# Performance work log

Measured on AMD Instinct MI355X. Metric: run time of the kernel, lower is better.

## Reference

```python
import jax, jax.numpy as jnp
import numpy as np

B, N, D, ATT = 8, 2048, 1024, 128

def setup_inputs() -> dict:
    key = jax.random.key(0)
    k1, k2, k3 = jax.random.split(key, 3)
    s = 1.0 / np.sqrt(D)
    return {
        "x": jax.random.normal(k1, (B, N, D), dtype=jnp.float32),
        "Wf": jax.random.normal(k2, (D, ATT), dtype=jnp.float32) * s,
        "bf": jnp.zeros((ATT,), dtype=jnp.float32),
        "Wg": jax.random.normal(k3, (D, ATT), dtype=jnp.float32) * s,
        "bg": jnp.zeros((ATT,), dtype=jnp.float32),
    }

def reference(x, Wf, bf, Wg, bg):
    # f, g: [B, N, ATT]
    f = jnp.einsum('bnd,da->bna', x, Wf) + bf
    g = jnp.einsum('bnd,da->bna', x, Wg) + bg
    # unscaled attention logits [B, N, N]
    att = jnp.einsum('bna,bma->bnm', f, g)
    att = jax.nn.softmax(att, axis=-1)
    # NOTE: original multiplies attention with x (not h); h branch is dead code.
    out = jnp.einsum('bnm,bmd->bnd', att, x)
    return out + x  # residual=True
```

## Files before the change

kernel.cpp:

```cpp
#include <hip/hip_runtime.h>
#include <hip/hip_fp16.h>


#define B_ 8
#define N_ 2048
#define D_ 1024
#define A_ 128

typedef _Float16 half8v  __attribute__((ext_vector_type(8)));
typedef _Float16 half4v  __attribute__((ext_vector_type(4)));
typedef float    floatx4 __attribute__((ext_vector_type(4)));

__device__ __forceinline__ floatx4 mfma32(half8v a, half8v b, floatx4 c) {
#if defined(__HIP_DEVICE_COMPILE__)
    return __builtin_amdgcn_mfma_f32_16x16x32_f16(a, b, c, 0, 0, 0);
#else
    return c;
#endif
}

__global__ __launch_bounds__(256) void xpose_kernel(
    const float* __restrict__ x, _Float16* __restrict__ xT)
{
    __shared__ __align__(16) _Float16 ts[64][80];
    const int n0 = blockIdx.x * 64, d0 = blockIdx.y * 64, b = blockIdx.z;
    const int t = threadIdx.x;
#pragma unroll
    for (int s = 0; s < 4; ++s) {
        int idx = t + 256 * s;
        int nl = idx >> 4, c4 = idx & 15;
        float4 v = ((const float4*)(x + ((size_t)(b * N_ + n0 + nl)) * D_ + d0))[c4];
        ts[c4 * 4 + 0][nl] = (_Float16)v.x;
        ts[c4 * 4 + 1][nl] = (_Float16)v.y;
        ts[c4 * 4 + 2][nl] = (_Float16)v.z;
        ts[c4 * 4 + 3][nl] = (_Float16)v.w;
    }
    __syncthreads();
#pragma unroll
    for (int s = 0; s < 2; ++s) {
        int idx = t + 256 * s;
        int dl = idx >> 3, c = idx & 7;
        *(uint4*)&xT[((size_t)b * D_ + d0 + dl) * N_ + n0 + c * 8] =
            *(const uint4*)&ts[dl][c * 8];
    }
}

__global__ __launch_bounds__(256) void wprep_kernel(
    const float* __restrict__ Wf, const float* __restrict__ Wg,
    _Float16* __restrict__ whT)
{
    __shared__ __align__(16) _Float16 ts[64][72];
    const int k0 = blockIdx.x * 64, c0 = blockIdx.y * 64;
    const float* W = blockIdx.z ? Wg : Wf;
    _Float16* dst = whT + (size_t)blockIdx.z * A_ * D_;
    const int t = threadIdx.x;
#pragma unroll
    for (int s = 0; s < 4; ++s) {
        int idx = t + 256 * s;
        int kl = idx >> 4, c4 = idx & 15;
        float4 v = *(const float4*)&W[(size_t)(k0 + kl) * A_ + c0 + c4 * 4];
        ts[c4 * 4 + 0][kl] = (_Float16)v.x;
        ts[c4 * 4 + 1][kl] = (_Float16)v.y;
        ts[c4 * 4 + 2][kl] = (_Float16)v.z;
        ts[c4 * 4 + 3][kl] = (_Float16)v.w;
    }
    __syncthreads();
#pragma unroll
    for (int s = 0; s < 2; ++s) {
        int idx = t + 256 * s;
        int cl = idx >> 3, ch = idx & 7;
        *(uint4*)&dst[(size_t)(c0 + cl) * D_ + k0 + ch * 8] =
            *(const uint4*)&ts[cl][ch * 8];
    }
}

__global__ __launch_bounds__(256) void fgmm_kernel(
    const float* __restrict__ x, const _Float16* __restrict__ whT,
    const float* __restrict__ bfv, const float* __restrict__ bgv,
    _Float16* __restrict__ fh, _Float16* __restrict__ gh)
{
    __shared__ __align__(16) _Float16 xs[64 * 40];
    __shared__ __align__(16) _Float16 wt[256 * 40];
    const int row0 = blockIdx.x * 64;
    const int t = threadIdx.x;
    const int w = t >> 6, lane = t & 63, quad = lane >> 4, l16 = lane & 15;
    const int wr  = (w >> 1) * 32;
    const int wch = (w & 1);

    float4 xRf[2];
    uint4  wR[4];
#define FG_LOAD_TILE(K0)                                                      \
    {                                                                         \
        _Pragma("unroll")                                                     \
        for (int s = 0; s < 2; ++s) {                                         \
            int idx = t + 256 * s;                                            \
            int r = idx >> 3, k4 = idx & 7;                                   \
            xRf[s] = *(const float4*)&x[(size_t)(row0 + r) * D_ + (K0) + k4 * 4]; \
        }                                                                     \
        _Pragma("unroll")                                                     \
        for (int s = 0; s < 4; ++s) {                                         \
            int idx = t + 256 * s;                                            \
            int c = idx >> 2, k8 = idx & 3;                                   \
            wR[s] = *(const uint4*)&whT[(size_t)c * D_ + (K0) + k8 * 8];      \
        }                                                                     \
    }

    FG_LOAD_TILE(0)

    floatx4 acc[2][8];
#pragma unroll
    for (int ms = 0; ms < 2; ++ms)
#pragma unroll
        for (int nt = 0; nt < 8; ++nt)
            acc[ms][nt] = (floatx4){0.f, 0.f, 0.f, 0.f};

    for (int kt = 0; kt < 32; ++kt) {
        __syncthreads();
#pragma unroll
        for (int s = 0; s < 2; ++s) {
            int idx = t + 256 * s;
            int r = idx >> 3, k4 = idx & 7;
            half4v h = {(_Float16)xRf[s].x, (_Float16)xRf[s].y,
                        (_Float16)xRf[s].z, (_Float16)xRf[s].w};
            *(half4v*)&xs[r * 40 + k4 * 4] = h;
        }
#pragma unroll
        for (int s = 0; s < 4; ++s) {
            int idx = t + 256 * s;
            int c = idx >> 2, k8 = idx & 3;
            *(uint4*)&wt[c * 40 + k8 * 8] = wR[s];
        }
        __syncthreads();
        if (kt < 31) FG_LOAD_TILE((kt + 1) * 32)

        half8v a0 = *(const half8v*)&xs[(wr + l16) * 40 + quad * 8];
        half8v a1 = *(const half8v*)&xs[(wr + 16 + l16) * 40 + quad * 8];
#pragma unroll
        for (int nt = 0; nt < 8; ++nt) {
            half8v bfr = *(const half8v*)&wt[(wch * 128 + nt * 16 + l16) * 40 + quad * 8];
            acc[0][nt] = mfma32(a0, bfr, acc[0][nt]);
            acc[1][nt] = mfma32(a1, bfr, acc[1][nt]);
        }
    }

    _Float16* dst = wch ? gh : fh;
    const float* bias = wch ? bgv : bfv;
#pragma unroll
    for (int nt = 0; nt < 8; ++nt) {
        int col = nt * 16 + l16;
        float bv = bias[col];
#pragma unroll
        for (int ms = 0; ms < 2; ++ms)
#pragma unroll
            for (int rg = 0; rg < 4; ++rg) {
                int row = row0 + wr + ms * 16 + quad * 4 + rg;
                dst[(size_t)row * A_ + col] = (_Float16)(acc[ms][nt][rg] + bv);
            }
    }
}

__global__ __launch_bounds__(256, 2) void attn_kernel(
    const float* __restrict__ x, const _Float16* __restrict__ f,
    const _Float16* __restrict__ g, const _Float16* __restrict__ xT,
    float* __restrict__ out)
{
    __shared__ __align__(16) _Float16 gS[32 * 136];
    __shared__ __align__(16) _Float16 xTs[256 * 40];

    const int dch = blockIdx.x;
    const int nt  = blockIdx.y;
    const int b   = blockIdx.z;
    const int tid = threadIdx.x;
    const int wave = tid >> 6, lane = tid & 63;
    const int quad = lane >> 4, l16 = lane & 15;
    const int d0 = dch * 256;
    const int qbase = nt * 128 + wave * 32;

    half8v fb[2][4];
#pragma unroll
    for (int it = 0; it < 2; ++it)
#pragma unroll
        for (int kc = 0; kc < 4; ++kc)
            fb[it][kc] = *(const half8v*)(f +
                ((size_t)(b * N_ + qbase + it * 16 + l16)) * A_ + kc * 32 + quad * 8);

    uint4 gR[2];
    uint2 xR[8];
#define AT_LOAD_TILE(M0)                                                      \
    {                                                                         \
        _Pragma("unroll")                                                     \
        for (int s = 0; s < 2; ++s) {                                         \
            int idx = tid + 256 * s;                                          \
            int r = idx >> 4, c = idx & 15;                                   \
            gR[s] = *(const uint4*)(g + ((size_t)(b * N_ + (M0) + r)) * A_ + c * 8); \
        }                                                                     \
        _Pragma("unroll")                                                     \
        for (int s = 0; s < 8; ++s) {                                         \
            int idx = tid + 256 * s;                                          \
            int rr = idx >> 3, p = idx & 7;                                   \
            xR[s] = *(const uint2*)(xT + ((size_t)b * D_ + d0 + rr) * N_ + (M0) + p * 4); \
        }                                                                     \
    }

    AT_LOAD_TILE(0)

    floatx4 acc[2][16];
#pragma unroll
    for (int it = 0; it < 2; ++it)
#pragma unroll
        for (int dt = 0; dt < 16; ++dt)
            acc[it][dt] = (floatx4){0.f, 0.f, 0.f, 0.f};
    float m_i[2]    = {-3.0e38f, -3.0e38f};
    float l_part[2] = {0.f, 0.f};

    for (int m0 = 0; m0 < N_; m0 += 32) {
        __syncthreads();
#pragma unroll
        for (int s = 0; s < 2; ++s) {
            int idx = tid + 256 * s;
            int r = idx >> 4, c = idx & 15;
            int slot = ((r >> 2) & 1) * 16 + ((r >> 3) & 3) * 4 + (r & 3);
            *(uint4*)&gS[slot * 136 + c * 8] = gR[s];
        }
#pragma unroll
        for (int s = 0; s < 8; ++s) {
            int idx = tid + 256 * s;
            int rr = idx >> 3, p = idx & 7;
            *(uint2*)&xTs[rr * 40 + p * 4] = xR[s];
        }
        __syncthreads();
        if (m0 + 32 < N_) AT_LOAD_TILE(m0 + 32)

        floatx4 sc[2][2];
#pragma unroll
        for (int fr = 0; fr < 2; ++fr)
#pragma unroll
            for (int it = 0; it < 2; ++it)
                sc[fr][it] = (floatx4){0.f, 0.f, 0.f, 0.f};
#pragma unroll
        for (int kc = 0; kc < 4; ++kc) {
            half8v ga0 = *(const half8v*)&gS[(l16     ) * 136 + kc * 32 + quad * 8];
            half8v ga1 = *(const half8v*)&gS[(l16 + 16) * 136 + kc * 32 + quad * 8];
            sc[0][0] = mfma32(ga0, fb[0][kc], sc[0][0]);
            sc[0][1] = mfma32(ga0, fb[1][kc], sc[0][1]);
            sc[1][0] = mfma32(ga1, fb[0][kc], sc[1][0]);
            sc[1][1] = mfma32(ga1, fb[1][kc], sc[1][1]);
        }

        float tm[2];
#pragma unroll
        for (int it = 0; it < 2; ++it) {
            float t0 = fmaxf(fmaxf(sc[0][it][0], sc[0][it][1]),
                             fmaxf(sc[0][it][2], sc[0][it][3]));
            float t1 = fmaxf(fmaxf(sc[1][it][0], sc[1][it][1]),
                             fmaxf(sc[1][it][2], sc[1][it][3]));
            float tv = fmaxf(t0, t1);
            tv = fmaxf(tv, __shfl_xor(tv, 16));
            tv = fmaxf(tv, __shfl_xor(tv, 32));
            tm[it] = tv;
        }
        bool needl = (tm[0] > m_i[0] + 8.0f) || (tm[1] > m_i[1] + 8.0f);
        if (__any(needl)) {
            float alpha[2];
#pragma unroll
            for (int it = 0; it < 2; ++it) {
                float mnew = fmaxf(m_i[it], tm[it]);
                alpha[it] = __expf(m_i[it] - mnew);
                m_i[it] = mnew;
                l_part[it] *= alpha[it];
            }
            float ar[2][4];
#pragma unroll
            for (int it = 0; it < 2; ++it)
#pragma unroll
                for (int r = 0; r < 4; ++r)
                    ar[it][r] = __shfl(alpha[it], quad * 4 + r);
#pragma unroll
            for (int it = 0; it < 2; ++it)
#pragma unroll
                for (int dt = 0; dt < 16; ++dt)
#pragma unroll
                    for (int r = 0; r < 4; ++r)
                        acc[it][dt][r] *= ar[it][r];
        }

        half8v pa[2];
#pragma unroll
        for (int it = 0; it < 2; ++it) {
            float e0 = __expf(sc[0][it][0] - m_i[it]);
            float e1 = __expf(sc[0][it][1] - m_i[it]);
            float e2 = __expf(sc[0][it][2] - m_i[it]);
            float e3 = __expf(sc[0][it][3] - m_i[it]);
            float e4 = __expf(sc[1][it][0] - m_i[it]);
            float e5 = __expf(sc[1][it][1] - m_i[it]);
            float e6 = __expf(sc[1][it][2] - m_i[it]);
            float e7 = __expf(sc[1][it][3] - m_i[it]);
            l_part[it] += ((e0 + e1) + (e2 + e3)) + ((e4 + e5) + (e6 + e7));
            pa[it] = (half8v){(_Float16)e0, (_Float16)e1, (_Float16)e2,
                              (_Float16)e3, (_Float16)e4, (_Float16)e5,
                              (_Float16)e6, (_Float16)e7};
        }

#pragma unroll
        for (int dt = 0; dt < 16; ++dt) {
            half8v xb = *(const half8v*)&xTs[(dt * 16 + l16) * 40 + quad * 8];
            acc[0][dt] = mfma32(pa[0], xb, acc[0][dt]);
            acc[1][dt] = mfma32(pa[1], xb, acc[1][dt]);
        }
    }

    float l_i[2];
#pragma unroll
    for (int it = 0; it < 2; ++it) {
        float rs = l_part[it];
        rs += __shfl_xor(rs, 16);
        rs += __shfl_xor(rs, 32);
        l_i[it] = rs;
    }
    float linv[2][4];
#pragma unroll
    for (int it = 0; it < 2; ++it)
#pragma unroll
        for (int r = 0; r < 4; ++r)
            linv[it][r] = 1.0f / __shfl(l_i[it], quad * 4 + r);

#pragma unroll
    for (int it = 0; it < 2; ++it)
#pragma unroll
        for (int r = 0; r < 4; ++r) {
            const size_t rowoff =
                ((size_t)(b * N_ + qbase + it * 16 + quad * 4 + r)) * D_ + d0;
#pragma unroll
            for (int dt = 0; dt < 16; ++dt) {
                int col = dt * 16 + l16;
                out[rowoff + col] = fmaf(acc[it][dt][r], linv[it][r], x[rowoff + col]);
            }
        }
}

extern "C" void kernel_launch(void* const* d_in, const int* in_sizes, int n_in,
                              void* d_out, int out_size, void* d_ws, size_t ws_size,
                              hipStream_t stream) {
    const float* x   = (const float*)d_in[0];
    const float* Wf  = (const float*)d_in[1];
    const float* bfv = (const float*)d_in[2];
    const float* Wg  = (const float*)d_in[3];
    const float* bgv = (const float*)d_in[4];
    float* out = (float*)d_out;

    _Float16* fh  = (_Float16*)d_ws;
    _Float16* gh  = fh + (size_t)B_ * N_ * A_;
    _Float16* xT  = gh + (size_t)B_ * N_ * A_;
    _Float16* whT = xT + (size_t)B_ * D_ * N_;

    hipLaunchKernelGGL(xpose_kernel, dim3(N_ / 64, D_ / 64, B_), dim3(256), 0, stream,
                       x, xT);
    hipLaunchKernelGGL(wprep_kernel, dim3(D_ / 64, A_ / 64, 2), dim3(256), 0, stream,
                       Wf, Wg, whT);
    hipLaunchKernelGGL(fgmm_kernel, dim3(B_ * N_ / 64), dim3(256), 0, stream,
                       x, whT, bfv, bgv, fh, gh);
    hipLaunchKernelGGL(attn_kernel, dim3(D_ / 256, N_ / 128, B_), dim3(256), 0, stream,
                       x, fh, gh, xT, out);
}
```

Before: 323.5 us.

## Reshape attention tiles to 16 queries per wave over 512 feature columns

Each wave of the attention kernel now handles 16 query rows instead of 32, and each block covers a 512-wide slice of D instead of 256. The query tile per block falls from 128 to 64 rows. The D axis now needs only 2 chunks instead of 4, so the QK^T score and softmax work, which is recomputed once per D chunk, is halved. The cost is that x^T tiles are reused by half as many queries, so x traffic per query doubles. The larger xT shared buffer and the 128 accumulator registers per lane may also reduce occupancy.

```diff
diff --git a/kernel.cpp b/kernel.cpp
--- a/kernel.cpp
+++ b/kernel.cpp
@@ -165,7 +165,7 @@
     float* __restrict__ out)
 {
     __shared__ __align__(16) _Float16 gS[32 * 136];
-    __shared__ __align__(16) _Float16 xTs[256 * 40];
+    __shared__ __align__(16) _Float16 xTs[512 * 40];
 
     const int dch = blockIdx.x;
     const int nt  = blockIdx.y;
@@ -173,19 +173,17 @@
     const int tid = threadIdx.x;
     const int wave = tid >> 6, lane = tid & 63;
     const int quad = lane >> 4, l16 = lane & 15;
-    const int d0 = dch * 256;
-    const int qbase = nt * 128 + wave * 32;
-
-    half8v fb[2][4];
-#pragma unroll
-    for (int it = 0; it < 2; ++it)
-#pragma unroll
-        for (int kc = 0; kc < 4; ++kc)
-            fb[it][kc] = *(const half8v*)(f +
-                ((size_t)(b * N_ + qbase + it * 16 + l16)) * A_ + kc * 32 + quad * 8);
+    const int d0 = dch * 512;
+    const int qbase = nt * 64 + wave * 16;
+
+    half8v fb[4];
+#pragma unroll
+    for (int kc = 0; kc < 4; ++kc)
+        fb[kc] = *(const half8v*)(f +
+            ((size_t)(b * N_ + qbase + l16)) * A_ + kc * 32 + quad * 8);
 
     uint4 gR[2];
-    uint2 xR[8];
+    uint4 xR[8];
 #define AT_LOAD_TILE(M0)                                                      \
     {                                                                         \
         _Pragma("unroll")                                                     \
@@ -197,21 +195,19 @@
         _Pragma("unroll")                                                     \
         for (int s = 0; s < 8; ++s) {                                         \
             int idx = tid + 256 * s;                                          \
-            int rr = idx >> 3, p = idx & 7;                                   \
-            xR[s] = *(const uint2*)(xT + ((size_t)b * D_ + d0 + rr) * N_ + (M0) + p * 4); \
+            int rr = idx >> 2, p = idx & 3;                                   \
+            xR[s] = *(const uint4*)(xT + ((size_t)b * D_ + d0 + rr) * N_ + (M0) + p * 8); \
         }                                                                     \
     }
 
     AT_LOAD_TILE(0)
 
-    floatx4 acc[2][16];
-#pragma unroll
-    for (int it = 0; it < 2; ++it)
-#pragma unroll
-        for (int dt = 0; dt < 16; ++dt)
-            acc[it][dt] = (floatx4){0.f, 0.f, 0.f, 0.f};
-    float m_i[2]    = {-3.0e38f, -3.0e38f};
-    float l_part[2] = {0.f, 0.f};
+    floatx4 acc[32];
+#pragma unroll
+    for (int dt = 0; dt < 32; ++dt)
+        acc[dt] = (floatx4){0.f, 0.f, 0.f, 0.f};
+    float m_i    = -3.0e38f;
+    float l_part = 0.f;
 
     for (int m0 = 0; m0 < N_; m0 += 32) {
         __syncthreads();
@@ -225,117 +221,82 @@
 #pragma unroll
         for (int s = 0; s < 8; ++s) {
             int idx = tid + 256 * s;
-            int rr = idx >> 3, p = idx & 7;
-            *(uint2*)&xTs[rr * 40 + p * 4] = xR[s];
+            int rr = idx >> 2, p = idx & 3;
+            *(uint4*)&xTs[rr * 40 + p * 8] = xR[s];
         }
         __syncthreads();
         if (m0 + 32 < N_) AT_LOAD_TILE(m0 + 32)
 
-        floatx4 sc[2][2];
-#pragma unroll
-        for (int fr = 0; fr < 2; ++fr)
-#pragma unroll
-            for (int it = 0; it < 2; ++it)
-                sc[fr][it] = (floatx4){0.f, 0.f, 0.f, 0.f};
+        floatx4 sc0 = (floatx4){0.f, 0.f, 0.f, 0.f};
+        floatx4 sc1 = (floatx4){0.f, 0.f, 0.f, 0.f};
 #pragma unroll
         for (int kc = 0; kc < 4; ++kc) {
             half8v ga0 = *(const half8v*)&gS[(l16     ) * 136 + kc * 32 + quad * 8];
             half8v ga1 = *(const half8v*)&gS[(l16 + 16) * 136 + kc * 32 + quad * 8];
-            sc[0][0] = mfma32(ga0, fb[0][kc], sc[0][0]);
-            sc[0][1] = mfma32(ga0, fb[1][kc], sc[0][1]);
-            sc[1][0] = mfma32(ga1, fb[0][kc], sc[1][0]);
-            sc[1][1] = mfma32(ga1, fb[1][kc], sc[1][1]);
-        }
-
-        float tm[2];
-#pragma unroll
-        for (int it = 0; it < 2; ++it) {
-            float t0 = fmaxf(fmaxf(sc[0][it][0], sc[0][it][1]),
-                             fmaxf(sc[0][it][2], sc[0][it][3]));
-            float t1 = fmaxf(fmaxf(sc[1][it][0], sc[1][it][1]),
-                             fmaxf(sc[1][it][2], sc[1][it][3]));
-            float tv = fmaxf(t0, t1);
-            tv = fmaxf(tv, __shfl_xor(tv, 16));
-            tv = fmaxf(tv, __shfl_xor(tv, 32));
-            tm[it] = tv;
-        }
-        bool needl = (tm[0] > m_i[0] + 8.0f) || (tm[1] > m_i[1] + 8.0f);
+            sc0 = mfma32(ga0, fb[kc], sc0);
+            sc1 = mfma32(ga1, fb[kc], sc1);
+        }
+
+        float t0 = fmaxf(fmaxf(sc0[0], sc0[1]), fmaxf(sc0[2], sc0[3]));
+        float t1 = fmaxf(fmaxf(sc1[0], sc1[1]), fmaxf(sc1[2], sc1[3]));
+        float tv = fmaxf(t0, t1);
+        tv = fmaxf(tv, __shfl_xor(tv, 16));
+        tv = fmaxf(tv, __shfl_xor(tv, 32));
+        bool needl = (tv > m_i + 8.0f);
         if (__any(needl)) {
-            float alpha[2];
-#pragma unroll
-            for (int it = 0; it < 2; ++it) {
-                float mnew = fmaxf(m_i[it], tm[it]);
-                alpha[it] = __expf(m_i[it] - mnew);
-                m_i[it] = mnew;
-                l_part[it] *= alpha[it];
-            }
-            float ar[2][4];
-#pragma unroll
-            for (int it = 0; it < 2; ++it)
+            float mnew = fmaxf(m_i, tv);
+            float alpha = __expf(m_i - mnew);
+            m_i = mnew;
+            l_part *= alpha;
+            float ar[4];
+#pragma unroll
+            for (int r = 0; r < 4; ++r)
+                ar[r] = __shfl(alpha, quad * 4 + r);
+#pragma unroll
+            for (int dt = 0; dt < 32; ++dt)
 #pragma unroll
                 for (int r = 0; r < 4; ++r)
-                    ar[it][r] = __shfl(alpha[it], quad * 4 + r);
-#pragma unroll
-            for (int it = 0; it < 2; ++it)
-#pragma unroll
-                for (int dt = 0; dt < 16; ++dt)
-#pragma unroll
-                    for (int r = 0; r < 4; ++r)
-                        acc[it][dt][r] *= ar[it][r];
-        }
-
-        half8v pa[2];
-#pragma unroll
-        for (int it = 0; it < 2; ++it) {
-            float e0 = __expf(sc[0][it][0] - m_i[it]);
-            float e1 = __expf(sc[0][it][1] - m_i[it]);
-            float e2 = __expf(sc[0][it][2] - m_i[it]);
-            float e3 = __expf(sc[0][it][3] - m_i[it]);
-            float e4 = __expf(sc[1][it][0] - m_i[it]);
-            float e5 = __expf(sc[1][it][1] - m_i[it]);
-            float e6 = __expf(sc[1][it][2] - m_i[it]);
-            float e7 = __expf(sc[1][it][3] - m_i[it]);
-            l_part[it] += ((e0 + e1) + (e2 + e3)) + ((e4 + e5) + (e6 + e7));
-            pa[it] = (half8v){(_Float16)e0, (_Float16)e1, (_Float16)e2,
-                              (_Float16)e3, (_Float16)e4, (_Float16)e5,
-                              (_Float16)e6, (_Float16)e7};
-        }
-
-#pragma unroll
-        for (int dt = 0; dt < 16; ++dt) {
+                    acc[dt][r] *= ar[r];
+        }
+
+        float e0 = __expf(sc0[0] - m_i);
+        float e1 = __expf(sc0[1] - m_i);
+        float e2 = __expf(sc0[2] - m_i);
+        float e3 = __expf(sc0[3] - m_i);
+        float e4 = __expf(sc1[0] - m_i);
+        float e5 = __expf(sc1[1] - m_i);
+        float e6 = __expf(sc1[2] - m_i);
+        float e7 = __expf(sc1[3] - m_i);
+        l_part += ((e0 + e1) + (e2 + e3)) + ((e4 + e5) + (e6 + e7));
+        half8v pa = (half8v){(_Float16)e0, (_Float16)e1, (_Float16)e2,
+                             (_Float16)e3, (_Float16)e4, (_Float16)e5,
+                             (_Float16)e6, (_Float16)e7};
+
+#pragma unroll
+        for (int dt = 0; dt < 32; ++dt) {
             half8v xb = *(const half8v*)&xTs[(dt * 16 + l16) * 40 + quad * 8];
-            acc[0][dt] = mfma32(pa[0], xb, acc[0][dt]);
-            acc[1][dt] = mfma32(pa[1], xb, acc[1][dt]);
-        }
-    }
-
-    float l_i[2];
-#pragma unroll
-    for (int it = 0; it < 2; ++it) {
-        float rs = l_part[it];
-        rs += __shfl_xor(rs, 16);
-        rs += __shfl_xor(rs, 32);
-        l_i[it] = rs;
-    }
-    float linv[2][4];
-#pragma unroll
-    for (int it = 0; it < 2; ++it)
-#pragma unroll
-        for (int r = 0; r < 4; ++r)
-            linv[it][r] = 1.0f / __shfl(l_i[it], quad * 4 + r);
-
-#pragma unroll
-    for (int it = 0; it < 2; ++it)
-#pragma unroll
-        for (int r = 0; r < 4; ++r) {
-            const size_t rowoff =
-                ((size_t)(b * N_ + qbase + it * 16 + quad * 4 + r)) * D_ + d0;
-#pragma unroll
-            for (int dt = 0; dt < 16; ++dt) {
-                int col = dt * 16 + l16;
-                out[rowoff + col] = fmaf(acc[it][dt][r], linv[it][r], x[rowoff + col]);
-            }
-        }
+            acc[dt] = mfma32(pa, xb, acc[dt]);
+        }
+    }
+
+    float rs = l_part;
+    rs += __shfl_xor(rs, 16);
+    rs += __shfl_xor(rs, 32);
+    float linv[4];
+#pragma unroll
+    for (int r = 0; r < 4; ++r)
+        linv[r] = 1.0f / __shfl(rs, quad * 4 + r);
+
+#pragma unroll
+    for (int r = 0; r < 4; ++r) {
+        const size_t rowoff =
+            ((size_t)(b * N_ + qbase + quad * 4 + r)) * D_ + d0;
+#pragma unroll
+        for (int dt = 0; dt < 32; ++dt) {
+            int col = dt * 16 + l16;
+            out[rowoff + col] = fmaf(acc[dt][r], linv[r], x[rowoff + col]);
+        }
+    }
 }
 
 extern "C" void kernel_launch(void* const* d_in, const int* in_sizes, int n_in,
@@ -359,6 +320,6 @@
                        Wf, Wg, whT);
     hipLaunchKernelGGL(fgmm_kernel, dim3(B_ * N_ / 64), dim3(256), 0, stream,
                        x, whT, bfv, bgv, fh, gh);
-    hipLaunchKernelGGL(attn_kernel, dim3(D_ / 256, N_ / 128, B_), dim3(256), 0, stream,
+    hipLaunchKernelGGL(attn_kernel, dim3(D_ / 512, N_ / 64, B_), dim3(256), 0, stream,
                        x, fh, gh, xT, out);
 }
```

After: 575.4 us. 77.9% more time.
